# Kernel tuning notes

Hardware: AMD Instinct MI355X
Metric: run time of the kernel (lower is better)

The kernel has to match this reference:

```python
import jax, jax.numpy as jnp
import numpy as np

CONTEXT_SIZE = 256  # hardcoded in source; scale = context_size**-0.5, not head_size
EMBED_DIM = 384
HEAD_SIZE = 64
BATCH = 512
SEQ = 256


def setup_inputs() -> dict:
    key = jax.random.key(0)
    ks = jax.random.split(key, 7)
    s = 1.0 / np.sqrt(EMBED_DIM)
    return {
        "x": jax.random.normal(ks[0], (BATCH, SEQ, EMBED_DIM), jnp.float32),
        "Wq": jax.random.uniform(ks[1], (EMBED_DIM, HEAD_SIZE), jnp.float32, -s, s),
        "bq": jax.random.uniform(ks[2], (HEAD_SIZE,), jnp.float32, -s, s),
        "Wk": jax.random.uniform(ks[3], (EMBED_DIM, HEAD_SIZE), jnp.float32, -s, s),
        "bk": jax.random.uniform(ks[4], (HEAD_SIZE,), jnp.float32, -s, s),
        "Wv": jax.random.uniform(ks[5], (EMBED_DIM, HEAD_SIZE), jnp.float32, -s, s),
        "bv": jax.random.uniform(ks[6], (HEAD_SIZE,), jnp.float32, -s, s),
    }


def reference(x, Wq, bq, Wk, bk, Wv, bv):
    # x: [B, T, D]
    T = x.shape[1]
    q = x @ Wq + bq          # [B, T, H]
    k = x @ Wk + bk          # [B, T, H]
    v = x @ Wv + bv          # [B, T, H]
    scale = CONTEXT_SIZE ** (-0.5)  # faithful: source scales by context_size, not head_size
    scores = jnp.einsum("bth,bsh->bts", q, k) * scale  # [B, T, T]
    causal = jnp.tril(jnp.ones((T, T), dtype=bool))
    scores = jnp.where(causal, scores, -jnp.inf)
    attn = jax.nn.softmax(scores, axis=-1)
    # dropout omitted (eval mode / deterministic reference)
    return jnp.einsum("bts,bsh->bth", attn, v)  # [B, T, H]
```

## Files before the change

### kernel.cpp

```cpp
#include <hip/hip_runtime.h>
#include <hip/hip_bf16.h>
#include <stdint.h>

#define B_ 512
#define T_ 256
#define D_ 384
#define H_ 64

typedef __attribute__((ext_vector_type(8))) short bf16x8;
typedef __attribute__((ext_vector_type(4))) float f32x4;
typedef __attribute__((ext_vector_type(16))) float f32x16;

__device__ __forceinline__ unsigned short f2bf(float f) {
  union { float f; unsigned int u; } a; a.f = f;
  unsigned int r = (a.u + 0x7FFFu + ((a.u >> 16) & 1u)) >> 16;
  return (unsigned short)r;
}

__device__ __forceinline__ unsigned int pkbf(float lo, float hi) {
  unsigned int r;
  asm("v_cvt_pk_bf16_f32 %0, %1, %2" : "=v"(r) : "v"(lo), "v"(hi));
  return r;
}

__global__ void prep_wt(const float* __restrict__ Wq, const float* __restrict__ Wk,
                        const float* __restrict__ Wv, unsigned short* __restrict__ wt) {
  int idx = blockIdx.x * 256 + threadIdx.x;
  if (idx >= 192 * 384) return;
  int n = idx / 384, k = idx - n * 384;
  int sel = n >> 6, c = n & 63;
  const float* W = (sel == 0) ? Wq : ((sel == 1) ? Wk : Wv);
  wt[idx] = f2bf(W[k * 64 + c]);
}

__global__ __launch_bounds__(512) void attn_fused(
    const float* __restrict__ x, const float* __restrict__ bq,
    const float* __restrict__ bk, const float* __restrict__ bv,
    const unsigned short* __restrict__ wt, float* __restrict__ out) {
  extern __shared__ char smem[];
  const int tid = threadIdx.x;
  const int b = blockIdx.x;
  const int wv = tid >> 6, lane = tid & 63;
  const int lo4 = lane & 15, hi4 = lane >> 4;
  const int lo5 = lane & 31, hi5 = lane >> 5;

  const float* xb = x + (size_t)b * T_ * D_;

  f32x4 acc[2][12];
#pragma unroll
  for (int rt = 0; rt < 2; ++rt)
#pragma unroll
    for (int ct = 0; ct < 12; ++ct) acc[rt][ct] = (f32x4)0.0f;

  const int row0 = 32 * wv + lo4;

  for (int half = 0; half < 2; ++half) {
#pragma unroll
    for (int i = 0; i < 9; ++i) {
      int u = tid + 512 * i;
      int n = u / 24;
      int mp = u - n * 24;
      int m = mp ^ (n & 7);
      const uint4* src = reinterpret_cast<const uint4*>(wt + n * 384 + half * 192 + 8 * m);
      *reinterpret_cast<uint4*>(smem + 16 * u) = *src;
    }
    __syncthreads();
#pragma unroll
    for (int ks6 = 0; ks6 < 6; ++ks6) {
      int ks = half * 6 + ks6;
      bf16x8 afr[2];
#pragma unroll
      for (int rt = 0; rt < 2; ++rt) {
        const float* p = xb + (row0 + 16 * rt) * D_ + 32 * ks + 8 * hi4;
        float4 f0 = *reinterpret_cast<const float4*>(p);
        float4 f1 = *reinterpret_cast<const float4*>(p + 4);
        union { bf16x8 v; unsigned int w[4]; } A;
        A.w[0] = pkbf(f0.x, f0.y); A.w[1] = pkbf(f0.z, f0.w);
        A.w[2] = pkbf(f1.x, f1.y); A.w[3] = pkbf(f1.z, f1.w);
        afr[rt] = A.v;
      }
#pragma unroll
      for (int ct = 0; ct < 12; ++ct) {
        int n = 16 * ct + lo4;
        int kbyte = (64 * ks6 + 16 * hi4) ^ ((n & 7) << 4);
        bf16x8 bw = *reinterpret_cast<const bf16x8*>(smem + n * 384 + kbyte);
        acc[0][ct] = __builtin_amdgcn_mfma_f32_16x16x32_bf16(afr[0], bw, acc[0][ct], 0, 0, 0);
        acc[1][ct] = __builtin_amdgcn_mfma_f32_16x16x32_bf16(afr[1], bw, acc[1][ct], 0, 0, 0);
      }
    }
    __syncthreads();
  }

#pragma unroll
  for (int ct = 0; ct < 12; ++ct) {
    int n = 16 * ct + lo4;
    float bias = (ct < 4) ? bq[n] : ((ct < 8) ? bk[n - 64] : bv[n - 128]);
#pragma unroll
    for (int rt = 0; rt < 2; ++rt) {
      int rowb = 32 * wv + 16 * rt + 4 * hi4;
#pragma unroll
      for (int r = 0; r < 4; ++r) {
        int row = rowb + r;
        unsigned short v = f2bf(acc[rt][ct][r] + bias);
        if (ct < 4) {
          int h = n;
          *reinterpret_cast<unsigned short*>(smem + row * 128 + ((2 * h) ^ ((row & 7) << 4))) = v;
        } else if (ct < 8) {
          int h = n - 64;
          *reinterpret_cast<unsigned short*>(smem + 32768 + row * 128 + ((2 * h) ^ ((row & 7) << 4))) = v;
        } else {
          int h = n - 128;
          *reinterpret_cast<unsigned short*>(smem + 65536 + h * 512 + ((2 * row) ^ ((h & 7) << 4))) = v;
        }
      }
    }
  }
  __syncthreads();

  const float cexp = 0.09016844005555897f;

  bf16x8 qf[4];
  {
    int row = 32 * wv + lo5;
#pragma unroll
    for (int s = 0; s < 4; ++s)
      qf[s] = *reinterpret_cast<const bf16x8*>(
          smem + row * 128 + (((32 * s + 16 * hi5)) ^ ((row & 7) << 4)));
  }

  f32x16 o0 = (f32x16)0.0f, o1 = (f32x16)0.0f;
  float lsum = 0.0f;

  for (int kb = 0; kb <= wv; ++kb) {
    f32x16 st = (f32x16)0.0f;
    {
      int row = 32 * kb + lo5;
#pragma unroll
      for (int s = 0; s < 4; ++s) {
        bf16x8 kf = *reinterpret_cast<const bf16x8*>(
            smem + 32768 + row * 128 + (((32 * s + 16 * hi5)) ^ ((row & 7) << 4)));
        st = __builtin_amdgcn_mfma_f32_32x32x16_bf16(kf, qf[s], st, 0, 0, 0);
      }
    }
    float p[16];
#pragma unroll
    for (int r = 0; r < 16; ++r) {
      float e = exp2f(cexp * st[r]);
      if (kb == wv) {
        int keyl = (r & 3) + 8 * (r >> 2) + 4 * hi5;
        if (keyl > lo5) e = 0.0f;
      }
      p[r] = e;
      lsum += e;
    }

    union { bf16x8 v; unsigned int w[4]; } A0, A1;
    {
      unsigned int X0 = pkbf(p[0], p[1]),  X1 = pkbf(p[2], p[3]);
      unsigned int Y0 = pkbf(p[4], p[5]),  Y1 = pkbf(p[6], p[7]);
      unsigned int X0p = (unsigned int)__shfl_xor((int)X0, 32);
      unsigned int X1p = (unsigned int)__shfl_xor((int)X1, 32);
      unsigned int Y0p = (unsigned int)__shfl_xor((int)Y0, 32);
      unsigned int Y1p = (unsigned int)__shfl_xor((int)Y1, 32);
      A0.w[0] = hi5 ? Y0p : X0;
      A0.w[1] = hi5 ? Y1p : X1;
      A0.w[2] = hi5 ? Y0  : X0p;
      A0.w[3] = hi5 ? Y1  : X1p;
      unsigned int Z0 = pkbf(p[8], p[9]),   Z1 = pkbf(p[10], p[11]);
      unsigned int W0 = pkbf(p[12], p[13]), W1 = pkbf(p[14], p[15]);
      unsigned int Z0p = (unsigned int)__shfl_xor((int)Z0, 32);
      unsigned int Z1p = (unsigned int)__shfl_xor((int)Z1, 32);
      unsigned int W0p = (unsigned int)__shfl_xor((int)W0, 32);
      unsigned int W1p = (unsigned int)__shfl_xor((int)W1, 32);
      A1.w[0] = hi5 ? W0p : Z0;
      A1.w[1] = hi5 ? W1p : Z1;
      A1.w[2] = hi5 ? W0  : Z0p;
      A1.w[3] = hi5 ? W1  : Z1p;
    }
#pragma unroll
    for (int s2 = 0; s2 < 2; ++s2) {
      bf16x8 pa = s2 ? A1.v : A0.v;
      int kk = 32 * kb + 16 * s2 + 8 * hi5;
#pragma unroll
      for (int ht = 0; ht < 2; ++ht) {
        int h = 32 * ht + lo5;
        bf16x8 vf = *reinterpret_cast<const bf16x8*>(
            smem + 65536 + h * 512 + (((2 * kk)) ^ ((h & 7) << 4)));
        if (ht == 0) o0 = __builtin_amdgcn_mfma_f32_32x32x16_bf16(pa, vf, o0, 0, 0, 0);
        else         o1 = __builtin_amdgcn_mfma_f32_32x32x16_bf16(pa, vf, o1, 0, 0, 0);
      }
    }
  }

  lsum += __shfl_xor(lsum, 32);
  float inv = 1.0f / lsum;
  float* ob = out + (size_t)b * T_ * H_;
#pragma unroll
  for (int r = 0; r < 16; ++r) {
    int ridx = (r & 3) + 8 * (r >> 2) + 4 * hi5;
    float invr = __shfl(inv, ridx);
    int row = 32 * wv + ridx;
    ob[row * H_ + lo5]      = o0[r] * invr;
    ob[row * H_ + 32 + lo5] = o1[r] * invr;
  }
}

extern "C" void kernel_launch(void* const* d_in, const int* in_sizes, int n_in,
                              void* d_out, int out_size, void* d_ws, size_t ws_size,
                              hipStream_t stream) {
  const float* x  = (const float*)d_in[0];
  const float* Wq = (const float*)d_in[1];
  const float* bq = (const float*)d_in[2];
  const float* Wk = (const float*)d_in[3];
  const float* bk = (const float*)d_in[4];
  const float* Wv = (const float*)d_in[5];
  const float* bv = (const float*)d_in[6];
  unsigned short* wt = (unsigned short*)d_ws;
  float* out = (float*)d_out;

  prep_wt<<<288, 256, 0, stream>>>(Wq, Wk, Wv, wt);
  attn_fused<<<B_, 512, 98304, stream>>>(x, bq, bk, bv, wt, out);
}
```

Measured before the change: 65.71 us.

## Process two batches per 1024-thread block sharing the staged weight tiles

Each block now handles two batch elements using 16 waves, so the bf16 weight tile loaded into shared memory serves twice as many rows per load. The Q/K/V shared-memory layout is reorganized so Q is read into registers first and its region is reused for K, with extra barriers, and shared memory per block grows to 128 KiB. This halves the number of weight staging passes, but 1024-thread blocks with large LDS may reduce occupancy and register budget per thread (launch bounds 1024 caps VGPRs), risking spills given the 24 f32x4 accumulators.

Result: slower. 133.6 us (+103.3%).

```diff
diff --git a/kernel.cpp b/kernel.cpp
--- a/kernel.cpp
+++ b/kernel.cpp
@@ -33,18 +33,20 @@
   wt[idx] = f2bf(W[k * 64 + c]);
 }
 
-__global__ __launch_bounds__(512) void attn_fused(
+__global__ __launch_bounds__(1024) void attn_fused(
     const float* __restrict__ x, const float* __restrict__ bq,
     const float* __restrict__ bk, const float* __restrict__ bv,
     const unsigned short* __restrict__ wt, float* __restrict__ out) {
   extern __shared__ char smem[];
   const int tid = threadIdx.x;
-  const int b = blockIdx.x;
   const int wv = tid >> 6, lane = tid & 63;
   const int lo4 = lane & 15, hi4 = lane >> 4;
   const int lo5 = lane & 31, hi5 = lane >> 5;
-
-  const float* xb = x + (size_t)b * T_ * D_;
+  const int bb = wv >> 3;
+  const int qw = wv & 7;
+  const size_t batch = 2 * (size_t)blockIdx.x + bb;
+
+  const float* xb = x + batch * T_ * D_;
 
   f32x4 acc[2][12];
 #pragma unroll
@@ -52,17 +54,17 @@
 #pragma unroll
     for (int ct = 0; ct < 12; ++ct) acc[rt][ct] = (f32x4)0.0f;
 
-  const int row0 = 32 * wv + lo4;
-
   for (int half = 0; half < 2; ++half) {
 #pragma unroll
-    for (int i = 0; i < 9; ++i) {
-      int u = tid + 512 * i;
-      int n = u / 24;
-      int mp = u - n * 24;
-      int m = mp ^ (n & 7);
-      const uint4* src = reinterpret_cast<const uint4*>(wt + n * 384 + half * 192 + 8 * m);
-      *reinterpret_cast<uint4*>(smem + 16 * u) = *src;
+    for (int i = 0; i < 5; ++i) {
+      int u = tid + 1024 * i;
+      if (u < 4608) {
+        int n = u / 24;
+        int mp = u - n * 24;
+        int m = mp ^ (n & 7);
+        const uint4* src = reinterpret_cast<const uint4*>(wt + n * 384 + half * 192 + 8 * m);
+        *reinterpret_cast<uint4*>(smem + 16 * u) = *src;
+      }
     }
     __syncthreads();
 #pragma unroll
@@ -71,7 +73,7 @@
       bf16x8 afr[2];
 #pragma unroll
       for (int rt = 0; rt < 2; ++rt) {
-        const float* p = xb + (row0 + 16 * rt) * D_ + 32 * ks + 8 * hi4;
+        const float* p = xb + (size_t)(32 * qw + 16 * rt + lo4) * D_ + 32 * ks + 8 * hi4;
         float4 f0 = *reinterpret_cast<const float4*>(p);
         float4 f1 = *reinterpret_cast<const float4*>(p + 4);
         union { bf16x8 v; unsigned int w[4]; } A;
@@ -91,26 +93,55 @@
     __syncthreads();
   }
 
-#pragma unroll
-  for (int ct = 0; ct < 12; ++ct) {
+  char* qbase = smem + bb * 32768;
+#pragma unroll
+  for (int ct = 0; ct < 4; ++ct) {
     int n = 16 * ct + lo4;
-    float bias = (ct < 4) ? bq[n] : ((ct < 8) ? bk[n - 64] : bv[n - 128]);
+    float bias = bq[n];
 #pragma unroll
     for (int rt = 0; rt < 2; ++rt) {
-      int rowb = 32 * wv + 16 * rt + 4 * hi4;
+      int rowb = 32 * qw + 16 * rt + 4 * hi4;
+#pragma unroll
+      for (int r = 0; r < 4; ++r) {
+        int row = rowb + r;
+        *reinterpret_cast<unsigned short*>(
+            qbase + row * 128 + ((2 * n) ^ ((row & 7) << 4))) = f2bf(acc[rt][ct][r] + bias);
+      }
+    }
+  }
+  __syncthreads();
+
+  bf16x8 qf[4];
+  {
+    int row = 32 * qw + lo5;
+#pragma unroll
+    for (int s = 0; s < 4; ++s)
+      qf[s] = *reinterpret_cast<const bf16x8*>(
+          qbase + row * 128 + (((32 * s + 16 * hi5)) ^ ((row & 7) << 4)));
+  }
+  __syncthreads();
+
+  char* kbase = smem + bb * 32768;
+  char* vbase = smem + 65536 + bb * 32768;
+#pragma unroll
+  for (int ct = 4; ct < 12; ++ct) {
+    int n = 16 * ct + lo4;
+    float bias = (ct < 8) ? bk[n - 64] : bv[n - 128];
+#pragma unroll
+    for (int rt = 0; rt < 2; ++rt) {
+      int rowb = 32 * qw + 16 * rt + 4 * hi4;
 #pragma unroll
       for (int r = 0; r < 4; ++r) {
         int row = rowb + r;
         unsigned short v = f2bf(acc[rt][ct][r] + bias);
-        if (ct < 4) {
-          int h = n;
-          *reinterpret_cast<unsigned short*>(smem + row * 128 + ((2 * h) ^ ((row & 7) << 4))) = v;
-        } else if (ct < 8) {
+        if (ct < 8) {
           int h = n - 64;
-          *reinterpret_cast<unsigned short*>(smem + 32768 + row * 128 + ((2 * h) ^ ((row & 7) << 4))) = v;
+          *reinterpret_cast<unsigned short*>(
+              kbase + row * 128 + ((2 * h) ^ ((row & 7) << 4))) = v;
         } else {
           int h = n - 128;
-          *reinterpret_cast<unsigned short*>(smem + 65536 + h * 512 + ((2 * row) ^ ((h & 7) << 4))) = v;
+          *reinterpret_cast<unsigned short*>(
+              vbase + h * 512 + ((2 * row) ^ ((h & 7) << 4))) = v;
         }
       }
     }
@@ -118,27 +149,18 @@
   __syncthreads();
 
   const float cexp = 0.09016844005555897f;
-
-  bf16x8 qf[4];
-  {
-    int row = 32 * wv + lo5;
-#pragma unroll
-    for (int s = 0; s < 4; ++s)
-      qf[s] = *reinterpret_cast<const bf16x8*>(
-          smem + row * 128 + (((32 * s + 16 * hi5)) ^ ((row & 7) << 4)));
-  }
 
   f32x16 o0 = (f32x16)0.0f, o1 = (f32x16)0.0f;
   float lsum = 0.0f;
 
-  for (int kb = 0; kb <= wv; ++kb) {
+  for (int kb = 0; kb <= qw; ++kb) {
     f32x16 st = (f32x16)0.0f;
     {
       int row = 32 * kb + lo5;
 #pragma unroll
       for (int s = 0; s < 4; ++s) {
         bf16x8 kf = *reinterpret_cast<const bf16x8*>(
-            smem + 32768 + row * 128 + (((32 * s + 16 * hi5)) ^ ((row & 7) << 4)));
+            kbase + row * 128 + (((32 * s + 16 * hi5)) ^ ((row & 7) << 4)));
         st = __builtin_amdgcn_mfma_f32_32x32x16_bf16(kf, qf[s], st, 0, 0, 0);
       }
     }
@@ -146,7 +168,7 @@
 #pragma unroll
     for (int r = 0; r < 16; ++r) {
       float e = exp2f(cexp * st[r]);
-      if (kb == wv) {
+      if (kb == qw) {
         int keyl = (r & 3) + 8 * (r >> 2) + 4 * hi5;
         if (keyl > lo5) e = 0.0f;
       }
@@ -185,7 +207,7 @@
       for (int ht = 0; ht < 2; ++ht) {
         int h = 32 * ht + lo5;
         bf16x8 vf = *reinterpret_cast<const bf16x8*>(
-            smem + 65536 + h * 512 + (((2 * kk)) ^ ((h & 7) << 4)));
+            vbase + h * 512 + (((2 * kk)) ^ ((h & 7) << 4)));
         if (ht == 0) o0 = __builtin_amdgcn_mfma_f32_32x32x16_bf16(pa, vf, o0, 0, 0, 0);
         else         o1 = __builtin_amdgcn_mfma_f32_32x32x16_bf16(pa, vf, o1, 0, 0, 0);
       }
@@ -194,12 +216,12 @@
 
   lsum += __shfl_xor(lsum, 32);
   float inv = 1.0f / lsum;
-  float* ob = out + (size_t)b * T_ * H_;
+  float* ob = out + batch * T_ * H_;
 #pragma unroll
   for (int r = 0; r < 16; ++r) {
     int ridx = (r & 3) + 8 * (r >> 2) + 4 * hi5;
     float invr = __shfl(inv, ridx);
-    int row = 32 * wv + ridx;
+    int row = 32 * qw + ridx;
     ob[row * H_ + lo5]      = o0[r] * invr;
     ob[row * H_ + 32 + lo5] = o1[r] * invr;
   }
@@ -219,5 +241,5 @@
   float* out = (float*)d_out;
 
   prep_wt<<<288, 256, 0, stream>>>(Wq, Wk, Wv, wt);
-  attn_fused<<<B_, 512, 98304, stream>>>(x, bq, bk, bv, wt, out);
-}
+  attn_fused<<<B_ / 2, 1024, 131072, stream>>>(x, bq, bk, bv, wt, out);
+}
```
